# Optimization experiments

Measured on AMD Instinct MI355X. Metric: run time of the kernel, lower is better.

The kernel has to match this reference:

```python
import jax, jax.numpy as jnp
import numpy as np

N_NODES = 50000
IN_CH = 128
OUT_CH = 64
HID = 2 * OUT_CH  # 128
N_EDGES = 800000


def _glorot(key, shape):
    fan_in, fan_out = shape[0], shape[-1]
    lim = jnp.sqrt(6.0 / (fan_in + fan_out))
    return jax.random.uniform(key, shape, jnp.float32, -lim, lim)


def setup_inputs() -> dict:
    key = jax.random.key(0)
    ks = jax.random.split(key, 10)
    x = jax.random.normal(ks[0], (N_NODES, IN_CH), jnp.float32)
    edge_index = jax.random.randint(ks[1], (2, N_EDGES), 0, N_NODES, jnp.int32)
    return {
        "x": x,
        "edge_index": edge_index,
        "W1": _glorot(ks[2], (IN_CH, HID)),
        "a_src1": _glorot(ks[3], (HID,)),
        "a_dst1": _glorot(ks[4], (HID,)),
        "b1": jnp.zeros((HID,), jnp.float32),
        "W2": _glorot(ks[5], (HID, OUT_CH)),
        "a_src2": _glorot(ks[6], (OUT_CH,)),
        "a_dst2": _glorot(ks[7], (OUT_CH,)),
        "b2": jnp.zeros((OUT_CH,), jnp.float32),
    }


def _gat_conv(x, src, dst, W, a_src, a_dst, b, n_nodes):
    # Linear transform: [N, F_out]
    h = x @ W
    # Per-node attention halves (heads=1): alpha_i = <h_i, a>
    al_s = h @ a_src  # [N]
    al_d = h @ a_dst  # [N]
    # Edge scores with LeakyReLU(0.2), PyG default negative slope
    e = jax.nn.leaky_relu(al_s[src] + al_d[dst], negative_slope=0.2)
    # Segment softmax over incoming edges of each dst node
    m = jax.ops.segment_max(e, dst, num_segments=n_nodes)
    m = jnp.where(jnp.isfinite(m), m, 0.0)
    ex = jnp.exp(e - m[dst])
    denom = jax.ops.segment_sum(ex, dst, num_segments=n_nodes)
    alpha = ex / (denom[dst] + 1e-16)  # [E]
    # Weighted scatter-add aggregation
    out = jax.ops.segment_sum(h[src] * alpha[:, None], dst, num_segments=n_nodes)
    return out + b


def reference(x, edge_index, W1, a_src1, a_dst1, b1, W2, a_src2, a_dst2, b2):
    n = x.shape[0]
    # add_self_loops=True (PyG GATConv default)
    loops = jnp.arange(n, dtype=edge_index.dtype)
    src = jnp.concatenate([edge_index[0], loops])
    dst = jnp.concatenate([edge_index[1], loops])
    h = _gat_conv(x.astype(jnp.float32), src, dst, W1, a_src1, a_dst1, b1, n)
    h = jax.nn.relu(h)
    return _gat_conv(h, src, dst, W2, a_src2, a_dst2, b2, n)
```

## Files before the change

kernel.cpp:

```cpp
#include <hip/hip_runtime.h>
#include <hip/hip_bf16.h>

#define N_NODES 50000
#define IN_CH 128
#define HID 128
#define OUT_CH 64
#define N_EDGES 800000
#define N_TOT_EDGES (N_EDGES + N_NODES)
#define ET_PAD (N_TOT_EDGES + 3 * N_NODES)
#define MPAD 50048
#define NBX (MPAD / 16)
#define NBN ((N_NODES + 255) / 256)
#define NB_E ((N_EDGES + 255) / 256)
#define NB_ET ((N_TOT_EDGES + 255) / 256)
#define NB_CVT (NBX + 12)
#define NB_GEMM (MPAD / 64)

typedef float float4v __attribute__((ext_vector_type(4)));
typedef unsigned uint4v __attribute__((ext_vector_type(4)));
typedef __attribute__((ext_vector_type(8))) short bf16x8;
typedef __attribute__((ext_vector_type(4))) float f32x4;

__device__ __forceinline__ unsigned bf16_rne(float f) {
    unsigned u = __float_as_uint(f);
    return (u + 0x7fffu + ((u >> 16) & 1u)) >> 16;
}
__device__ __forceinline__ unsigned pack2(float a, float b) {
    return bf16_rne(a) | (bf16_rne(b) << 16);
}


__device__ __forceinline__ void count_body(int b, int t,
        const int* __restrict__ dst_row, int* __restrict__ cnt,
        unsigned short* __restrict__ rank, int e) {
    int i = b * 256 + t;
    if (i < e) {
        int d = __builtin_nontemporal_load(&dst_row[i]);
        rank[i] = (unsigned short)atomicAdd(&cnt[d], 1);
    }
}

__device__ __forceinline__ void cvt_body(int b, int t,
        const float* __restrict__ X, unsigned short* __restrict__ Xb,
        const float* __restrict__ W1, unsigned short* __restrict__ Wl1,
        const float* __restrict__ W2, unsigned short* __restrict__ Wl2, int M) {
    if (b < NBX) {
        const int kg = t >> 4, rl = t & 15;
        const int row = b * 16 + rl;
        float4 a = make_float4(0.f, 0.f, 0.f, 0.f), c = a;
        if (row < M) {
            a = *(const float4*)&X[(size_t)row * 128 + kg * 8];
            c = *(const float4*)&X[(size_t)row * 128 + kg * 8 + 4];
        }
        uint4 p;
        p.x = pack2(a.x, a.y); p.y = pack2(a.z, a.w);
        p.z = pack2(c.x, c.y); p.w = pack2(c.z, c.w);
        *(uint4*)&Xb[(size_t)b * 2048 + kg * 128 + rl * 8] = p;
        return;
    }
    const float* W; unsigned short* Wl; int N, bb;
    if (b < NBX + 8) { W = W1; Wl = Wl1; N = 128; bb = b - NBX; }
    else             { W = W2; Wl = Wl2; N = 64;  bb = b - NBX - 8; }
    const int tg = bb * 256 + t;
    if (tg >= 16 * N) return;
    const int kg = tg / N, col = tg & (N - 1);
    float v[8];
    #pragma unroll
    for (int j = 0; j < 8; ++j) v[j] = W[(size_t)(kg * 8 + j) * N + col];
    uint4 p;
    p.x = pack2(v[0], v[1]); p.y = pack2(v[2], v[3]);
    p.z = pack2(v[4], v[5]); p.w = pack2(v[6], v[7]);
    *(uint4*)&Wl[(size_t)tg * 8] = p;
}

__device__ __forceinline__ void fill_body(int b, int t,
        const int* __restrict__ ei, const int* __restrict__ off,
        const unsigned short* __restrict__ rank,
        int* __restrict__ csr, int e, int n) {
    int i = b * 256 + t;
    if (i < e) {
        int src = __builtin_nontemporal_load(&ei[i]);
        int dst = __builtin_nontemporal_load(&ei[e + i]);
        csr[off[dst] + rank[i]] = src;
    } else if (i < e + n) {
        int v = i - e;
        csr[off[v]] = v;
    }
}

template<int N>
__device__ __forceinline__ void gemm_body(int gb, int t,
        const unsigned short* __restrict__ Xb, const unsigned short* __restrict__ Wlg,
        const float* __restrict__ asrc, const float* __restrict__ adst,
        unsigned short* __restrict__ Hb, float* __restrict__ als,
        float* __restrict__ ald, int M, unsigned short* Wl) {
    constexpr int NF = N / 16;
    for (int i = t; i < N * 16; i += 256)
        ((uint4*)Wl)[i] = ((const uint4*)Wlg)[i];
    __syncthreads();

    const int lane = t & 63, w = t >> 6;
    const int rb = gb * 64 + w * 16;
    const int cl = lane & 15, g = lane >> 4;
    const unsigned short* __restrict__ Abase = Xb + (size_t)(rb >> 4) * 2048 + cl * 8;

    f32x4 acc[NF];
    #pragma unroll
    for (int n = 0; n < NF; ++n) acc[n] = (f32x4){0.f, 0.f, 0.f, 0.f};

    #pragma unroll
    for (int s = 0; s < 4; ++s) {
        bf16x8 af = *(const bf16x8*)(Abase + (s * 4 + g) * 128);
        #pragma unroll
        for (int n = 0; n < NF; ++n) {
            bf16x8 bf = *(const bf16x8*)(Wl + ((s * 4 + g) * N + n * 16 + cl) * 8);
            acc[n] = __builtin_amdgcn_mfma_f32_16x16x32_bf16(af, bf, acc[n], 0, 0, 0);
        }
    }

    float asv[NF], adv[NF];
    #pragma unroll
    for (int n = 0; n < NF; ++n) {
        asv[n] = asrc[n * 16 + cl];
        adv[n] = adst[n * 16 + cl];
    }

    #pragma unroll
    for (int r = 0; r < 4; ++r) {
        float ps = 0.f, pd = 0.f;
        #pragma unroll
        for (int n = 0; n < NF; ++n) {
            ps += acc[n][r] * asv[n];
            pd += acc[n][r] * adv[n];
        }
        #pragma unroll
        for (int mask = 1; mask < 16; mask <<= 1) {
            ps += __shfl_xor(ps, mask);
            pd += __shfl_xor(pd, mask);
        }
        const int row = rb + g * 4 + r;
        if (cl == 0 && row < M) { als[row] = ps; ald[row] = pd; }
    }

    #pragma unroll
    for (int r = 0; r < 4; ++r) {
        const int row = rb + g * 4 + r;
        if (row >= M) continue;
        #pragma unroll
        for (int n = 0; n < NF; ++n)
            Hb[(size_t)(n >> 1) * (size_t)M * 32 + (size_t)row * 32
               + (n & 1) * 16 + cl] = (unsigned short)bf16_rne(acc[n][r]);
    }
}


__global__ void k_init_cnt(int* cnt, int n) {
    int i = blockIdx.x * 256 + threadIdx.x;
    if (i < n) cnt[i] = 1;
}

__global__ __launch_bounds__(256) void k_par1(
        const int* __restrict__ ei, int* __restrict__ cnt,
        unsigned short* __restrict__ rank,
        const float* __restrict__ X, unsigned short* __restrict__ Xb,
        const float* __restrict__ W1, unsigned short* __restrict__ Wl1,
        const float* __restrict__ W2, unsigned short* __restrict__ Wl2, int M) {
    const int b = blockIdx.x, t = threadIdx.x;
    if (b < NB_E) count_body(b, t, ei + N_EDGES, cnt, rank, N_EDGES);
    else         cvt_body(b - NB_E, t, X, Xb, W1, Wl1, W2, Wl2, M);
}

__global__ void k_scan1(const int* __restrict__ cnt, int* __restrict__ off,
                        int* __restrict__ bsum, int n) {
    __shared__ int s[256];
    int t = threadIdx.x;
    int i = blockIdx.x * 256 + t;
    int v = (i < n) ? ((cnt[i] + 3) & ~3) : 0;
    s[t] = v;
    __syncthreads();
    for (int d = 1; d < 256; d <<= 1) {
        int x = (t >= d) ? s[t - d] : 0;
        __syncthreads();
        s[t] += x;
        __syncthreads();
    }
    if (i < n) off[i + 1] = s[t];
    if (t == 255) bsum[blockIdx.x] = s[255];
}

__global__ void k_scan2(int* __restrict__ bsum, int nb) {
    __shared__ int s[256];
    int t = threadIdx.x;
    int v = (t < nb) ? bsum[t] : 0;
    s[t] = v;
    __syncthreads();
    for (int d = 1; d < 256; d <<= 1) {
        int x = (t >= d) ? s[t - d] : 0;
        __syncthreads();
        s[t] += x;
        __syncthreads();
    }
    if (t < nb) bsum[t] = s[t] - v;
}

__global__ void k_scan3(int* __restrict__ off, const int* __restrict__ bsum, int n) {
    int i = blockIdx.x * 256 + threadIdx.x;
    if (i < n) off[i + 1] += bsum[blockIdx.x];
    if (i == 0) off[0] = 0;
}

__global__ __launch_bounds__(256) void k_par2(
        const int* __restrict__ ei, const int* __restrict__ off,
        const unsigned short* __restrict__ rank, int* __restrict__ csr,
        const unsigned short* __restrict__ Xb, const unsigned short* __restrict__ Wlg,
        const float* __restrict__ asrc, const float* __restrict__ adst,
        unsigned short* __restrict__ Hb, float* __restrict__ als,
        float* __restrict__ ald, int M) {
    __shared__ unsigned short Wl[16 * 128 * 8];
    const int b = blockIdx.x, t = threadIdx.x;
    if (b < NB_ET) fill_body(b, t, ei, off, rank, csr, N_EDGES, N_NODES);
    else gemm_body<HID>(b - NB_ET, t, Xb, Wlg, asrc, adst, Hb, als, ald, M, Wl);
}

__global__ __launch_bounds__(256) void gemm_mfma64(
        const unsigned short* __restrict__ Xb, const unsigned short* __restrict__ Wlg,
        const float* __restrict__ asrc, const float* __restrict__ adst,
        unsigned short* __restrict__ Hb, float* __restrict__ als,
        float* __restrict__ ald, int M) {
    __shared__ unsigned short Wl[16 * 64 * 8];
    gemm_body<OUT_CH>(blockIdx.x, threadIdx.x, Xb, Wlg, asrc, adst, Hb, als, ald, M, Wl);
}

template<bool PADZ>
__global__ __launch_bounds__(256) void k_edgew(
        const float* __restrict__ als, const float* __restrict__ ald,
        const int* __restrict__ off, const int* __restrict__ cnt,
        const int* __restrict__ csr,
        unsigned* __restrict__ ew, float* __restrict__ invden, int n) {
    const int fl = threadIdx.x & 15;
    const int v = blockIdx.x * 16 + (threadIdx.x >> 4);
    if (v >= n) return;
    const int start = off[v], end = start + cnt[v];
    const float aldv = ald[v];
    float s = 0.f;
    for (int j = start + fl; j < end; j += 16) {
        int src = __builtin_nontemporal_load(&csr[j]);
        float e = als[src] + aldv;
        e = e > 0.f ? e : 0.2f * e;
        unsigned r = bf16_rne(__expf(e));
        ew[j] = ((unsigned)src << 16) | r;
        s += __uint_as_float(r << 16);
    }
    if (PADZ) {
        const int pend = off[v + 1];
        for (int j = end + fl; j < pend; j += 16) ew[j] = 0;
    }
    #pragma unroll
    for (int d = 1; d < 16; d <<= 1) s += __shfl_xor(s, d);
    if (fl == 0) invden[v] = 1.f / (s + 1e-16f);
}

template<int F, bool RELU, bool PACKOUT>
__global__ __launch_bounds__(256) void k_spmm_b(
        const unsigned short* __restrict__ Hb, const unsigned* __restrict__ ew,
        const float* __restrict__ invden, const float* __restrict__ bias,
        const int* __restrict__ off, void* __restrict__ outv, int n) {
    constexpr int NCH = F / 32;
    const int chunk = blockIdx.x % NCH;
    const int v = (blockIdx.x / NCH) * 64 + (threadIdx.x >> 2);
    if (v >= n) return;
    const int q = threadIdx.x & 3;
    const int start = off[v], end = off[v + 1];
    const unsigned short* __restrict__ Hch = Hb + (size_t)chunk * (size_t)n * 32 + q * 8;

    float a0[8] = {}, a1[8] = {}, a2[8] = {}, a3[8] = {};

    #define GATB(E, A)                                                   \
        {                                                                \
            float w_ = __uint_as_float((E) << 16);                       \
            uint4 h_ = *(const uint4*)&Hch[(size_t)((E) >> 16) * 32];    \
            A[0] += w_ * __uint_as_float(h_.x << 16);                    \
            A[1] += w_ * __uint_as_float(h_.x & 0xffff0000u);            \
            A[2] += w_ * __uint_as_float(h_.y << 16);                    \
            A[3] += w_ * __uint_as_float(h_.y & 0xffff0000u);            \
            A[4] += w_ * __uint_as_float(h_.z << 16);                    \
            A[5] += w_ * __uint_as_float(h_.z & 0xffff0000u);            \
            A[6] += w_ * __uint_as_float(h_.w << 16);                    \
            A[7] += w_ * __uint_as_float(h_.w & 0xffff0000u);            \
        }
    #define GATB4(Q) GATB((Q).x, a0) GATB((Q).y, a1) GATB((Q).z, a2) GATB((Q).w, a3)

    int j = start;
    for (; j + 4 < end; j += 8) {
        uint4 eA = *(const uint4*)&ew[j];
        uint4 eB = *(const uint4*)&ew[j + 4];
        GATB4(eA)
        GATB4(eB)
    }
    if (j < end) {
        uint4 eA = *(const uint4*)&ew[j];
        GATB4(eA)
    }
    #undef GATB4
    #undef GATB

    const float inv = invden[v];
    const float* __restrict__ bp = bias + chunk * 32 + q * 8;
    float s[8];
    #pragma unroll
    for (int i = 0; i < 8; ++i) {
        s[i] = (a0[i] + a1[i] + a2[i] + a3[i]) * inv + bp[i];
        if (RELU) s[i] = fmaxf(s[i], 0.f);
    }

    if (PACKOUT) {
        unsigned short* Xb2 = (unsigned short*)outv;
        const int kg = chunk * 4 + q;
        uint4v p;
        p[0] = pack2(s[0], s[1]); p[1] = pack2(s[2], s[3]);
        p[2] = pack2(s[4], s[5]); p[3] = pack2(s[6], s[7]);
        __builtin_nontemporal_store(p,
            (uint4v*)&Xb2[(size_t)(v >> 4) * 2048 + kg * 128 + (v & 15) * 8]);
    } else {
        float* out = (float*)outv;
        float4v o0, o1;
        o0[0] = s[0]; o0[1] = s[1]; o0[2] = s[2]; o0[3] = s[3];
        o1[0] = s[4]; o1[1] = s[5]; o1[2] = s[6]; o1[3] = s[7];
        float* op = out + (size_t)v * F + chunk * 32 + q * 8;
        __builtin_nontemporal_store(o0, (float4v*)op);
        __builtin_nontemporal_store(o1, (float4v*)(op + 4));
    }
}


extern "C" void kernel_launch(void* const* d_in, const int* in_sizes, int n_in,
                              void* d_out, int out_size, void* d_ws, size_t ws_size,
                              hipStream_t stream) {
    const float* x     = (const float*)d_in[0];
    const int*   ei    = (const int*)d_in[1];
    const float* W1    = (const float*)d_in[2];
    const float* as1   = (const float*)d_in[3];
    const float* ad1   = (const float*)d_in[4];
    const float* b1    = (const float*)d_in[5];
    const float* W2    = (const float*)d_in[6];
    const float* as2   = (const float*)d_in[7];
    const float* ad2   = (const float*)d_in[8];
    const float* b2    = (const float*)d_in[9];
    float* out = (float*)d_out;

    const int Nn = N_NODES;

    char* ws = (char*)d_ws;
    size_t o = 0;
    auto carve = [&](size_t bytes) { char* p = ws + o; o = (o + bytes + 255) & ~(size_t)255; return p; };
    int*            off  = (int*)carve((Nn + 1) * sizeof(int));
    int*            cnt  = (int*)carve(Nn * sizeof(int));
    int*            bsum = (int*)carve(256 * sizeof(int));
    unsigned short* rank = (unsigned short*)carve((size_t)N_EDGES * sizeof(unsigned short));
    int*            csr  = (int*)carve((size_t)ET_PAD * sizeof(int));
    unsigned*       ew   = (unsigned*)carve((size_t)ET_PAD * sizeof(unsigned));
    unsigned short* h1b  = (unsigned short*)carve((size_t)Nn * HID * sizeof(unsigned short));
    unsigned short* h2b  = (unsigned short*)carve((size_t)Nn * OUT_CH * sizeof(unsigned short));
    unsigned short* Xb1  = (unsigned short*)carve((size_t)MPAD * 128 * sizeof(unsigned short));
    unsigned short* Xb2  = (unsigned short*)carve((size_t)MPAD * 128 * sizeof(unsigned short));
    unsigned short* Wl1  = (unsigned short*)carve(16 * 128 * 8 * sizeof(unsigned short));
    unsigned short* Wl2  = (unsigned short*)carve(16 * 64 * 8 * sizeof(unsigned short));
    float*          als  = (float*)carve(Nn * sizeof(float));
    float*          ald  = (float*)carve(Nn * sizeof(float));
    float*          invd = (float*)carve(Nn * sizeof(float));

    k_init_cnt<<<NBN, 256, 0, stream>>>(cnt, Nn);

    k_par1<<<NB_E + NB_CVT, 256, 0, stream>>>(
        ei, cnt, rank, x, Xb1, W1, Wl1, W2, Wl2, Nn);

    k_scan1<<<NBN, 256, 0, stream>>>(cnt, off, bsum, Nn);
    k_scan2<<<1, 256, 0, stream>>>(bsum, NBN);
    k_scan3<<<NBN, 256, 0, stream>>>(off, bsum, Nn);

    k_par2<<<NB_ET + NB_GEMM, 256, 0, stream>>>(
        ei, off, rank, csr, Xb1, Wl1, as1, ad1, h1b, als, ald, Nn);

    const int nbEW  = (Nn + 15) / 16;
    const int nbN64 = (Nn + 63) / 64;

    k_edgew<true><<<nbEW, 256, 0, stream>>>(als, ald, off, cnt, csr, ew, invd, Nn);
    k_spmm_b<HID, true, true><<<nbN64 * (HID / 32), 256, 0, stream>>>(
        h1b, ew, invd, b1, off, Xb2, Nn);

    gemm_mfma64<<<NB_GEMM, 256, 0, stream>>>(
        Xb2, Wl2, as2, ad2, h2b, als, ald, Nn);
    k_edgew<false><<<nbEW, 256, 0, stream>>>(als, ald, off, cnt, csr, ew, invd, Nn);
    k_spmm_b<OUT_CH, false, false><<<nbN64 * (OUT_CH / 32), 256, 0, stream>>>(
        h2b, ew, invd, b2, off, out, Nn);
}
```

Baseline: 162.7 us.

## Fuse X fp32-to-bf16 conversion into layer-1 GEMM and reschedule kernels

The layer-1 GEMM now reads fp32 X directly and converts it to bf16 in registers, so the separate conversion pass and the Xb1 buffer's write and reread are gone. The count init and weight conversion are merged into one small pre-kernel, and the layer-1 GEMM moves to run alongside edge counting instead of alongside CSR fill. The fill becomes its own kernel. The A-operand loads are now uncoalesced fp32 row reads, and the conversion arithmetic is repeated inside the GEMM.

```diff
diff --git a/kernel.cpp b/kernel.cpp
--- a/kernel.cpp
+++ b/kernel.cpp
@@ -9,11 +9,9 @@
 #define N_TOT_EDGES (N_EDGES + N_NODES)
 #define ET_PAD (N_TOT_EDGES + 3 * N_NODES)
 #define MPAD 50048
-#define NBX (MPAD / 16)
 #define NBN ((N_NODES + 255) / 256)
 #define NB_E ((N_EDGES + 255) / 256)
 #define NB_ET ((N_TOT_EDGES + 255) / 256)
-#define NB_CVT (NBX + 12)
 #define NB_GEMM (MPAD / 64)
 
 typedef float float4v __attribute__((ext_vector_type(4)));
@@ -27,6 +25,31 @@
 }
 __device__ __forceinline__ unsigned pack2(float a, float b) {
     return bf16_rne(a) | (bf16_rne(b) << 16);
+}
+
+__global__ __launch_bounds__(256) void k_pre(
+        int* __restrict__ cnt,
+        const float* __restrict__ W1, unsigned short* __restrict__ Wl1,
+        const float* __restrict__ W2, unsigned short* __restrict__ Wl2, int n) {
+    const int b = blockIdx.x, t = threadIdx.x;
+    if (b < NBN) {
+        int i = b * 256 + t;
+        if (i < n) cnt[i] = 1;
+        return;
+    }
+    const float* W; unsigned short* Wl; int N, bb;
+    if (b < NBN + 8) { W = W1; Wl = Wl1; N = 128; bb = b - NBN; }
+    else             { W = W2; Wl = Wl2; N = 64;  bb = b - NBN - 8; }
+    const int tg = bb * 256 + t;
+    if (tg >= 16 * N) return;
+    const int kg = tg / N, col = tg & (N - 1);
+    float v[8];
+    #pragma unroll
+    for (int j = 0; j < 8; ++j) v[j] = W[(size_t)(kg * 8 + j) * N + col];
+    uint4 p;
+    p.x = pack2(v[0], v[1]); p.y = pack2(v[2], v[3]);
+    p.z = pack2(v[4], v[5]); p.w = pack2(v[6], v[7]);
+    *(uint4*)&Wl[(size_t)tg * 8] = p;
 }
 
 
@@ -40,57 +63,10 @@
     }
 }
 
-__device__ __forceinline__ void cvt_body(int b, int t,
-        const float* __restrict__ X, unsigned short* __restrict__ Xb,
-        const float* __restrict__ W1, unsigned short* __restrict__ Wl1,
-        const float* __restrict__ W2, unsigned short* __restrict__ Wl2, int M) {
-    if (b < NBX) {
-        const int kg = t >> 4, rl = t & 15;
-        const int row = b * 16 + rl;
-        float4 a = make_float4(0.f, 0.f, 0.f, 0.f), c = a;
-        if (row < M) {
-            a = *(const float4*)&X[(size_t)row * 128 + kg * 8];
-            c = *(const float4*)&X[(size_t)row * 128 + kg * 8 + 4];
-        }
-        uint4 p;
-        p.x = pack2(a.x, a.y); p.y = pack2(a.z, a.w);
-        p.z = pack2(c.x, c.y); p.w = pack2(c.z, c.w);
-        *(uint4*)&Xb[(size_t)b * 2048 + kg * 128 + rl * 8] = p;
-        return;
-    }
-    const float* W; unsigned short* Wl; int N, bb;
-    if (b < NBX + 8) { W = W1; Wl = Wl1; N = 128; bb = b - NBX; }
-    else             { W = W2; Wl = Wl2; N = 64;  bb = b - NBX - 8; }
-    const int tg = bb * 256 + t;
-    if (tg >= 16 * N) return;
-    const int kg = tg / N, col = tg & (N - 1);
-    float v[8];
-    #pragma unroll
-    for (int j = 0; j < 8; ++j) v[j] = W[(size_t)(kg * 8 + j) * N + col];
-    uint4 p;
-    p.x = pack2(v[0], v[1]); p.y = pack2(v[2], v[3]);
-    p.z = pack2(v[4], v[5]); p.w = pack2(v[6], v[7]);
-    *(uint4*)&Wl[(size_t)tg * 8] = p;
-}
-
-__device__ __forceinline__ void fill_body(int b, int t,
-        const int* __restrict__ ei, const int* __restrict__ off,
-        const unsigned short* __restrict__ rank,
-        int* __restrict__ csr, int e, int n) {
-    int i = b * 256 + t;
-    if (i < e) {
-        int src = __builtin_nontemporal_load(&ei[i]);
-        int dst = __builtin_nontemporal_load(&ei[e + i]);
-        csr[off[dst] + rank[i]] = src;
-    } else if (i < e + n) {
-        int v = i - e;
-        csr[off[v]] = v;
-    }
-}
-
-template<int N>
+template<int N, bool AF32>
 __device__ __forceinline__ void gemm_body(int gb, int t,
-        const unsigned short* __restrict__ Xb, const unsigned short* __restrict__ Wlg,
+        const float* __restrict__ Xf, const unsigned short* __restrict__ Xb,
+        const unsigned short* __restrict__ Wlg,
         const float* __restrict__ asrc, const float* __restrict__ adst,
         unsigned short* __restrict__ Hb, float* __restrict__ als,
         float* __restrict__ ald, int M, unsigned short* Wl) {
@@ -102,15 +78,34 @@
     const int lane = t & 63, w = t >> 6;
     const int rb = gb * 64 + w * 16;
     const int cl = lane & 15, g = lane >> 4;
-    const unsigned short* __restrict__ Abase = Xb + (size_t)(rb >> 4) * 2048 + cl * 8;
 
     f32x4 acc[NF];
     #pragma unroll
     for (int n = 0; n < NF; ++n) acc[n] = (f32x4){0.f, 0.f, 0.f, 0.f};
 
+    const float* Xrow = nullptr;
+    const unsigned short* Abase = nullptr;
+    if constexpr (AF32) {
+        const int arow = (rb + cl < M) ? (rb + cl) : (M - 1);
+        Xrow = Xf + (size_t)arow * 128;
+    } else {
+        Abase = Xb + (size_t)(rb >> 4) * 2048 + cl * 8;
+    }
+
     #pragma unroll
     for (int s = 0; s < 4; ++s) {
-        bf16x8 af = *(const bf16x8*)(Abase + (s * 4 + g) * 128);
+        bf16x8 af;
+        if constexpr (AF32) {
+            const int k0 = (s * 4 + g) * 8;
+            float4 a = *(const float4*)&Xrow[k0];
+            float4 c = *(const float4*)&Xrow[k0 + 4];
+            uint4v uu;
+            uu[0] = pack2(a.x, a.y); uu[1] = pack2(a.z, a.w);
+            uu[2] = pack2(c.x, c.y); uu[3] = pack2(c.z, c.w);
+            af = __builtin_bit_cast(bf16x8, uu);
+        } else {
+            af = *(const bf16x8*)(Abase + (s * 4 + g) * 128);
+        }
         #pragma unroll
         for (int n = 0; n < NF; ++n) {
             bf16x8 bf = *(const bf16x8*)(Wl + ((s * 4 + g) * N + n * 16 + cl) * 8);
@@ -153,22 +148,19 @@
     }
 }
 
-
-__global__ void k_init_cnt(int* cnt, int n) {
-    int i = blockIdx.x * 256 + threadIdx.x;
-    if (i < n) cnt[i] = 1;
-}
-
 __global__ __launch_bounds__(256) void k_par1(
         const int* __restrict__ ei, int* __restrict__ cnt,
         unsigned short* __restrict__ rank,
-        const float* __restrict__ X, unsigned short* __restrict__ Xb,
-        const float* __restrict__ W1, unsigned short* __restrict__ Wl1,
-        const float* __restrict__ W2, unsigned short* __restrict__ Wl2, int M) {
+        const float* __restrict__ X, const unsigned short* __restrict__ Wl1,
+        const float* __restrict__ asrc, const float* __restrict__ adst,
+        unsigned short* __restrict__ Hb, float* __restrict__ als,
+        float* __restrict__ ald, int M) {
+    __shared__ unsigned short Wl[16 * 128 * 8];
     const int b = blockIdx.x, t = threadIdx.x;
-    if (b < NB_E) count_body(b, t, ei + N_EDGES, cnt, rank, N_EDGES);
-    else         cvt_body(b - NB_E, t, X, Xb, W1, Wl1, W2, Wl2, M);
-}
+    if (b < NB_E) { count_body(b, t, ei + N_EDGES, cnt, rank, N_EDGES); return; }
+    gemm_body<HID, true>(b - NB_E, t, X, nullptr, Wl1, asrc, adst, Hb, als, ald, M, Wl);
+}
+
 
 __global__ void k_scan1(const int* __restrict__ cnt, int* __restrict__ off,
                         int* __restrict__ bsum, int n) {
@@ -209,17 +201,18 @@
     if (i == 0) off[0] = 0;
 }
 
-__global__ __launch_bounds__(256) void k_par2(
-        const int* __restrict__ ei, const int* __restrict__ off,
-        const unsigned short* __restrict__ rank, int* __restrict__ csr,
-        const unsigned short* __restrict__ Xb, const unsigned short* __restrict__ Wlg,
-        const float* __restrict__ asrc, const float* __restrict__ adst,
-        unsigned short* __restrict__ Hb, float* __restrict__ als,
-        float* __restrict__ ald, int M) {
-    __shared__ unsigned short Wl[16 * 128 * 8];
-    const int b = blockIdx.x, t = threadIdx.x;
-    if (b < NB_ET) fill_body(b, t, ei, off, rank, csr, N_EDGES, N_NODES);
-    else gemm_body<HID>(b - NB_ET, t, Xb, Wlg, asrc, adst, Hb, als, ald, M, Wl);
+__global__ void k_fill2(const int* __restrict__ ei, const int* __restrict__ off,
+                        const unsigned short* __restrict__ rank,
+                        int* __restrict__ csr, int e, int n) {
+    int i = blockIdx.x * 256 + threadIdx.x;
+    if (i < e) {
+        int src = __builtin_nontemporal_load(&ei[i]);
+        int dst = __builtin_nontemporal_load(&ei[e + i]);
+        csr[off[dst] + rank[i]] = src;
+    } else if (i < e + n) {
+        int v = i - e;
+        csr[off[v]] = v;
+    }
 }
 
 __global__ __launch_bounds__(256) void gemm_mfma64(
@@ -228,7 +221,8 @@
         unsigned short* __restrict__ Hb, float* __restrict__ als,
         float* __restrict__ ald, int M) {
     __shared__ unsigned short Wl[16 * 64 * 8];
-    gemm_body<OUT_CH>(blockIdx.x, threadIdx.x, Xb, Wlg, asrc, adst, Hb, als, ald, M, Wl);
+    gemm_body<OUT_CH, false>(blockIdx.x, threadIdx.x, nullptr, Xb, Wlg,
+                             asrc, adst, Hb, als, ald, M, Wl);
 }
 
 template<bool PADZ>
@@ -361,7 +355,6 @@
     unsigned*       ew   = (unsigned*)carve((size_t)ET_PAD * sizeof(unsigned));
     unsigned short* h1b  = (unsigned short*)carve((size_t)Nn * HID * sizeof(unsigned short));
     unsigned short* h2b  = (unsigned short*)carve((size_t)Nn * OUT_CH * sizeof(unsigned short));
-    unsigned short* Xb1  = (unsigned short*)carve((size_t)MPAD * 128 * sizeof(unsigned short));
     unsigned short* Xb2  = (unsigned short*)carve((size_t)MPAD * 128 * sizeof(unsigned short));
     unsigned short* Wl1  = (unsigned short*)carve(16 * 128 * 8 * sizeof(unsigned short));
     unsigned short* Wl2  = (unsigned short*)carve(16 * 64 * 8 * sizeof(unsigned short));
@@ -369,17 +362,16 @@
     float*          ald  = (float*)carve(Nn * sizeof(float));
     float*          invd = (float*)carve(Nn * sizeof(float));
 
-    k_init_cnt<<<NBN, 256, 0, stream>>>(cnt, Nn);
-
-    k_par1<<<NB_E + NB_CVT, 256, 0, stream>>>(
-        ei, cnt, rank, x, Xb1, W1, Wl1, W2, Wl2, Nn);
+    k_pre<<<NBN + 12, 256, 0, stream>>>(cnt, W1, Wl1, W2, Wl2, Nn);
+
+    k_par1<<<NB_E + NB_GEMM, 256, 0, stream>>>(
+        ei, cnt, rank, x, Wl1, as1, ad1, h1b, als, ald, Nn);
 
     k_scan1<<<NBN, 256, 0, stream>>>(cnt, off, bsum, Nn);
     k_scan2<<<1, 256, 0, stream>>>(bsum, NBN);
     k_scan3<<<NBN, 256, 0, stream>>>(off, bsum, Nn);
 
-    k_par2<<<NB_ET + NB_GEMM, 256, 0, stream>>>(
-        ei, off, rank, csr, Xb1, Wl1, as1, ad1, h1b, als, ald, Nn);
+    k_fill2<<<NB_ET, 256, 0, stream>>>(ei, off, rank, csr, N_EDGES, Nn);
 
     const int nbEW  = (Nn + 15) / 16;
     const int nbN64 = (Nn + 63) / 64;
```

Result: no change. 162.7 us (+0.0%).
